# Performance work log

Hardware: AMD Instinct MI355X
Metric: run time of the kernel (lower is better)

## Reference

```python
import jax, jax.numpy as jnp
import numpy as np

N = 40962          # icosphere level-6 vertex count
E = 245772         # N * k (k=6 knn, directed)
MUL_IN = 8         # '8x0e + 8x1o' -> dim 8 + 24 = 32
MUL_OUT = 16       # '16x0e + 16x1o' -> dim 16 + 48 = 64
H = 64             # radial MLP hidden
WNUM = 4 * MUL_IN * MUL_OUT  # 512 per-edge TP weights (4 CG paths)
SQ3 = np.float32(np.sqrt(3.0))


def setup_inputs() -> dict:
    key = jax.random.key(0)
    ks = jax.random.split(key, 8)
    x = jax.random.normal(ks[0], (N, MUL_IN + 3 * MUL_IN), dtype=jnp.float32)
    pos = jax.random.normal(ks[1], (N, 3), dtype=jnp.float32)
    src = jax.random.randint(ks[2], (E,), 0, N)
    dst = jax.random.randint(ks[3], (E,), 0, N)
    edge_index = jnp.stack([src, dst]).astype(jnp.int32)
    W1 = jax.random.normal(ks[4], (1, H), dtype=jnp.float32)
    W2 = jax.random.normal(ks[5], (H, WNUM), dtype=jnp.float32)
    Ws = jax.random.normal(ks[6], (MUL_OUT, MUL_OUT), dtype=jnp.float32)
    k7, k8 = jax.random.split(ks[7])
    Wns = jax.random.normal(k7, (MUL_OUT, MUL_OUT), dtype=jnp.float32)
    Wg = jax.random.normal(k8, (MUL_OUT, MUL_OUT), dtype=jnp.float32)
    return {"x": x, "pos": pos, "edge_index": edge_index,
            "W1": W1, "W2": W2, "Ws": Ws, "Wns": Wns, "Wg": Wg}


def reference(x, pos, edge_index, W1, W2, Ws, Wns, Wg):
    src, dst = edge_index[0], edge_index[1]
    xs = x[:, :MUL_IN]                                  # (N, 8)  scalars (0e)
    xv = x[:, MUL_IN:].reshape(-1, MUL_IN, 3)           # (N, 8, 3) vectors (1o)

    # --- edge geometry + spherical harmonics (component-normalized, lmax=1) ---
    edge_vec = pos[dst] - pos[src]                      # (E, 3)
    edge_len = jnp.maximum(jnp.linalg.norm(edge_vec, axis=-1, keepdims=True), 1e-8)
    edge_dir = edge_vec / edge_len                      # (E, 3)
    Y1 = SQ3 * edge_dir                                 # l=1 SH; l=0 SH == 1

    # --- radial MLP -> per-edge tensor-product weights (shared_weights=False) ---
    h = jax.nn.silu(edge_len @ W1)                      # (E, H), fan_in = 1
    w = (h @ W2) * (1.0 / np.sqrt(np.float32(H)))       # (E, 512)
    wA, wB, wC, wD = [wi.reshape(-1, MUL_IN, MUL_OUT)
                      for wi in jnp.split(w, 4, axis=1)]

    xs_e = xs[src]                                      # (E, 8)   gather
    xv_e = xv[src]                                      # (E, 8, 3) gather
    norm = np.float32(1.0 / np.sqrt(2.0 * MUL_IN))      # path normalization

    # --- tensor product: 4 CG paths ---
    # 0e x 0e -> 0e  (CG = 1)
    pathA = jnp.einsum('eu,euw->ew', xs_e, wA)
    # 1o x 1o -> 0e  (CG_ij = delta_ij / sqrt(3))
    dot = jnp.einsum('eui,ei->eu', xv_e, Y1) * (1.0 / SQ3)
    pathB = jnp.einsum('eu,euw->ew', dot, wB)
    m_s = (pathA + pathB) * norm                        # (E, 16)
    # 0e x 1o -> 1o  (CG = identity)
    pathC = jnp.einsum('eu,euw->ew', xs_e, wC)[:, :, None] * Y1[:, None, :]
    # 1o x 0e -> 1o  (CG = identity)
    pathD = jnp.einsum('eui,euw->ewi', xv_e, wD)
    m_v = (pathC + pathD) * norm                        # (E, 16, 3)

    m = jnp.concatenate([m_s, m_v.reshape(-1, 3 * MUL_OUT)], axis=1)  # (E, 64)

    # --- scatter-add to destination nodes (index_add) ---
    out = jnp.zeros((x.shape[0], m.shape[1]), dtype=x.dtype).at[dst].add(m)

    # --- gated equivariant nonlinearity (o3.Linear with fan-in norm) ---
    lin_norm = np.float32(1.0 / np.sqrt(np.float32(MUL_OUT)))
    os_ = out[:, :MUL_OUT]                              # (N, 16)
    ov_ = out[:, MUL_OUT:].reshape(-1, MUL_OUT, 3)      # (N, 16, 3)
    s = jax.nn.silu(os_ @ Ws * lin_norm)                # (N, 16)
    ns = jnp.einsum('nui,uw->nwi', ov_, Wns) * lin_norm # (N, 16, 3)
    g = jax.nn.sigmoid(os_ @ Wg * lin_norm)             # (N, 16)
    gated = (g[:, :, None] * ns).reshape(-1, 3 * MUL_OUT)
    return jnp.concatenate([s, gated], axis=1)          # (N, 64)
```

## Files before the change

### kernel.cpp

```cpp
#include <hip/hip_runtime.h>
#include <math.h>

typedef _Float16 half8 __attribute__((ext_vector_type(8)));
typedef float floatx4 __attribute__((ext_vector_type(4)));

#define SQ3 1.7320508075688772f

__global__ __launch_bounds__(256) void prep_w2(const float* __restrict__ W2,
                                               _Float16* __restrict__ bw) {
    int t = blockIdx.x * 256 + threadIdx.x;
    if (t >= 32768) return;
    int i    = t & 7;
    int l    = (t >> 3) & 63;
    int s    = (t >> 9) & 1;
    int tt   = (t >> 10) & 7;
    int path = t >> 13;
    int k   = s * 32 + (l >> 4) * 8 + i;
    int col = path * 128 + tt * 16 + (l & 15);
    float scale = 0.03125f * (path == 2 ? SQ3 : 1.0f);
    bw[t] = (_Float16)(W2[k * 512 + col] * scale);
}

struct Pref {
    float4 xa, xb;
    float psx, psy, psz, pdx, pdy, pdz;
    int di;
};

__device__ __forceinline__ Pref issue_loads(int tile, int E,
        const int* __restrict__ ei, const float* __restrict__ x,
        const float* __restrict__ pos, int tid) {
    Pref p;
    int el = tid >> 2, q = tid & 3;
    int eg = tile * 64 + el;
    int ec = (eg < E) ? eg : (E - 1);
    int si = ei[ec];
    p.di = ei[E + ec];
    const float* xr = x + (size_t)si * 32 + q * 8;
    p.xa = *reinterpret_cast<const float4*>(xr);
    p.xb = *reinterpret_cast<const float4*>(xr + 4);
    const float* ps = pos + (size_t)si * 3;
    const float* pd = pos + (size_t)p.di * 3;
    p.psx = ps[0]; p.psy = ps[1]; p.psz = ps[2];
    p.pdx = pd[0]; p.pdy = pd[1]; p.pdz = pd[2];
    return p;
}

__global__ __launch_bounds__(256) void edge_kernel(
    const float* __restrict__ x, const float* __restrict__ pos,
    const int* __restrict__ ei, const float* __restrict__ W1,
    const _Float16* __restrict__ bw, float* __restrict__ out,
    int E, int ntiles)
{
    __shared__ float sW1[64];
    __shared__ __align__(16) float4 s_geo[64];
    __shared__ int s_dst[2][64];
    __shared__ __align__(16) float s_xs[64][12];
    __shared__ __align__(16) float s_xvp[3][64][12];
    __shared__ __align__(16) _Float16 s_hA[4][2][64][8];
    __shared__ __align__(16) _Float16 s_part[2][64][66];

    const int tid  = threadIdx.x;
    const int wave = tid >> 6;
    const int lane = tid & 63;

    if (tid < 64) sW1[tid] = W1[tid];

    half8 bfrag[8][2];
    {
        const half8* bsrc = (const half8*)bw;
        #pragma unroll
        for (int t = 0; t < 8; ++t)
            #pragma unroll
            for (int s = 0; s < 2; ++s)
                bfrag[t][s] = bsrc[(size_t)wave * 1024 + (t * 2 + s) * 64 + lane];
    }

    int tile = blockIdx.x;
    if (tile >= ntiles) return;
    Pref p = issue_loads(tile, E, ei, x, pos, tid);
    __syncthreads();

    int buf = 0;
    for (; tile < ntiles; tile += gridDim.x) {
        {
            int el = tid >> 2, q = tid & 3;
            float ex = p.pdx - p.psx;
            float ey = p.pdy - p.psy;
            float ez = p.pdz - p.psz;
            float len = fmaxf(sqrtf(ex * ex + ey * ey + ez * ez), 1e-8f);
            float inv = 1.0f / len;
            if (q == 0) {
                s_geo[el] = make_float4(ex * inv, ey * inv, ez * inv, len);
                s_dst[buf][el] = p.di;
                *(float4*)&s_xs[el][0] = p.xa;
                *(float4*)&s_xs[el][4] = p.xb;
            } else {
                int fb = (q - 1) * 8;
                float vals[8] = {p.xa.x, p.xa.y, p.xa.z, p.xa.w,
                                 p.xb.x, p.xb.y, p.xb.z, p.xb.w};
                #pragma unroll
                for (int i2 = 0; i2 < 8; ++i2) {
                    int flat = fb + i2;
                    int u  = (flat * 11) >> 5;
                    int ii = flat - 3 * u;
                    s_xvp[ii][el][u] = vals[i2];
                }
            }
            int sub = el >> 4;
            int l   = (q << 4) | (el & 15);
            #pragma unroll
            for (int s = 0; s < 2; ++s) {
                half8 ha;
                #pragma unroll
                for (int i = 0; i < 8; ++i) {
                    float z = len * sW1[s * 32 + q * 8 + i];
                    ha[i] = (_Float16)(z / (1.0f + __expf(-z)));
                }
                *(half8*)&s_hA[sub][s][l][0] = ha;
            }
        }
        __syncthreads();

        int nt = tile + gridDim.x;
        Pref pn;
        if (nt < ntiles) pn = issue_loads(nt, E, ei, x, pos, tid);

        const int wp  = lane & 15;
        const int er0 = (lane >> 4) * 4;
        #pragma unroll
        for (int sub = 0; sub < 4; ++sub) {
            half8 a0 = *(const half8*)&s_hA[sub][0][lane][0];
            half8 a1 = *(const half8*)&s_hA[sub][1][lane][0];
            floatx4 acc[8];
            #pragma unroll
            for (int t = 0; t < 8; ++t) {
                floatx4 z = {0.f, 0.f, 0.f, 0.f};
                z = __builtin_amdgcn_mfma_f32_16x16x32_f16(a0, bfrag[t][0], z, 0, 0, 0);
                acc[t] = __builtin_amdgcn_mfma_f32_16x16x32_f16(a1, bfrag[t][1], z, 0, 0, 0);
            }

            if (wave == 0) {
                #pragma unroll
                for (int r = 0; r < 4; ++r) {
                    int e = sub * 16 + er0 + r;
                    float4 x0 = *(const float4*)&s_xs[e][0];
                    float4 x1 = *(const float4*)&s_xs[e][4];
                    float m = x0.x*acc[0][r] + x0.y*acc[1][r] + x0.z*acc[2][r] + x0.w*acc[3][r]
                            + x1.x*acc[4][r] + x1.y*acc[5][r] + x1.z*acc[6][r] + x1.w*acc[7][r];
                    s_part[0][e][wp] = (_Float16)m;
                }
            } else if (wave == 1) {
                #pragma unroll
                for (int r = 0; r < 4; ++r) {
                    int e = sub * 16 + er0 + r;
                    float4 g = s_geo[e];
                    float m = 0.f;
                    #pragma unroll
                    for (int i = 0; i < 3; ++i) {
                        float4 v0 = *(const float4*)&s_xvp[i][e][0];
                        float4 v1 = *(const float4*)&s_xvp[i][e][4];
                        float gi = (i == 0) ? g.x : ((i == 1) ? g.y : g.z);
                        float d = v0.x*acc[0][r] + v0.y*acc[1][r] + v0.z*acc[2][r] + v0.w*acc[3][r]
                                + v1.x*acc[4][r] + v1.y*acc[5][r] + v1.z*acc[6][r] + v1.w*acc[7][r];
                        m += gi * d;
                    }
                    s_part[1][e][wp] = (_Float16)m;
                }
            } else if (wave == 2) {
                #pragma unroll
                for (int r = 0; r < 4; ++r) {
                    int e = sub * 16 + er0 + r;
                    float4 x0 = *(const float4*)&s_xs[e][0];
                    float4 x1 = *(const float4*)&s_xs[e][4];
                    float4 g = s_geo[e];
                    float cw = x0.x*acc[0][r] + x0.y*acc[1][r] + x0.z*acc[2][r] + x0.w*acc[3][r]
                             + x1.x*acc[4][r] + x1.y*acc[5][r] + x1.z*acc[6][r] + x1.w*acc[7][r];
                    s_part[0][e][16 + wp * 3 + 0] = (_Float16)(cw * g.x);
                    s_part[0][e][16 + wp * 3 + 1] = (_Float16)(cw * g.y);
                    s_part[0][e][16 + wp * 3 + 2] = (_Float16)(cw * g.z);
                }
            } else {
                #pragma unroll
                for (int r = 0; r < 4; ++r) {
                    int e = sub * 16 + er0 + r;
                    #pragma unroll
                    for (int i = 0; i < 3; ++i) {
                        float4 v0 = *(const float4*)&s_xvp[i][e][0];
                        float4 v1 = *(const float4*)&s_xvp[i][e][4];
                        float mi = v0.x*acc[0][r] + v0.y*acc[1][r] + v0.z*acc[2][r] + v0.w*acc[3][r]
                                 + v1.x*acc[4][r] + v1.y*acc[5][r] + v1.z*acc[6][r] + v1.w*acc[7][r];
                        s_part[1][e][16 + wp * 3 + i] = (_Float16)mi;
                    }
                }
            }
        }
        __syncthreads();

        {
            int c = tid & 63;
            int g = tid >> 6;
            #pragma unroll
            for (int k = 0; k < 16; ++k) {
                int e  = g * 16 + k;
                int eg = tile * 64 + e;
                if (eg < E) {
                    float v = (float)s_part[0][e][c] + (float)s_part[1][e][c];
                    atomicAdd(out + (size_t)s_dst[buf][e] * 64 + c, v);
                }
            }
        }
        p = pn;
        buf ^= 1;
    }
}

__global__ __launch_bounds__(256) void node_kernel(
    float* __restrict__ out, const float* __restrict__ Ws,
    const float* __restrict__ Wns, const float* __restrict__ Wg, int N)
{
    int n = blockIdx.x * 256 + threadIdx.x;
    if (n >= N) return;
    float* row = out + (size_t)n * 64;

    float os[16], ov[48];
    #pragma unroll
    for (int q = 0; q < 4; ++q) {
        float4 v = *reinterpret_cast<const float4*>(row + q * 4);
        os[q*4+0]=v.x; os[q*4+1]=v.y; os[q*4+2]=v.z; os[q*4+3]=v.w;
    }
    #pragma unroll
    for (int q = 0; q < 12; ++q) {
        float4 v = *reinterpret_cast<const float4*>(row + 16 + q * 4);
        ov[q*4+0]=v.x; ov[q*4+1]=v.y; ov[q*4+2]=v.z; ov[q*4+3]=v.w;
    }

    float sres[16], gres[16];
    #pragma unroll
    for (int w = 0; w < 16; ++w) {
        float a = 0.f, b = 0.f;
        #pragma unroll
        for (int u = 0; u < 16; ++u) {
            float o_u = os[u];
            a += o_u * Ws[u * 16 + w];
            b += o_u * Wg[u * 16 + w];
        }
        a *= 0.25f; b *= 0.25f;
        sres[w] = a / (1.0f + __expf(-a));
        gres[w] = 1.0f / (1.0f + __expf(-b));
    }

    float gated[48];
    #pragma unroll
    for (int w = 0; w < 16; ++w) {
        float n0 = 0.f, n1 = 0.f, n2 = 0.f;
        #pragma unroll
        for (int u = 0; u < 16; ++u) {
            float wn = Wns[u * 16 + w];
            n0 += ov[u*3+0] * wn;
            n1 += ov[u*3+1] * wn;
            n2 += ov[u*3+2] * wn;
        }
        float gw = gres[w] * 0.25f;
        gated[w*3+0] = n0 * gw;
        gated[w*3+1] = n1 * gw;
        gated[w*3+2] = n2 * gw;
    }

    #pragma unroll
    for (int q = 0; q < 4; ++q) {
        float4 v = make_float4(sres[q*4+0], sres[q*4+1], sres[q*4+2], sres[q*4+3]);
        *reinterpret_cast<float4*>(row + q * 4) = v;
    }
    #pragma unroll
    for (int q = 0; q < 12; ++q) {
        float4 v = make_float4(gated[q*4+0], gated[q*4+1], gated[q*4+2], gated[q*4+3]);
        *reinterpret_cast<float4*>(row + 16 + q * 4) = v;
    }
}

extern "C" void kernel_launch(void* const* d_in, const int* in_sizes, int n_in,
                              void* d_out, int out_size, void* d_ws, size_t ws_size,
                              hipStream_t stream) {
    const float* x   = (const float*)d_in[0];
    const float* pos = (const float*)d_in[1];
    const int*   ei  = (const int*)d_in[2];
    const float* W1  = (const float*)d_in[3];
    const float* W2  = (const float*)d_in[4];
    const float* Ws  = (const float*)d_in[5];
    const float* Wns = (const float*)d_in[6];
    const float* Wg  = (const float*)d_in[7];

    int N = in_sizes[0] / 32;
    int E = in_sizes[2] / 2;
    int ntiles = (E + 63) / 64;
    float* out = (float*)d_out;
    _Float16* bw = (_Float16*)d_ws;

    hipMemsetAsync(out, 0, (size_t)N * 64 * sizeof(float), stream);
    prep_w2<<<128, 256, 0, stream>>>(W2, bw);
    int nblk = ntiles < 1024 ? ntiles : 1024;
    edge_kernel<<<nblk, 256, 0, stream>>>(x, pos, ei, W1, bw, out, E, ntiles);
    node_kernel<<<(N + 255) / 256, 256, 0, stream>>>(out, Ws, Wns, Wg, N);
}
```

Before: 115.1 us.

## Split each TP path across two waves with 512-thread blocks

Doubles the block to 8 waves so each CG path is handled by two waves, each owning half of the input multiplicity (4 of 8 u-channels). This halves the per-wave B-fragment registers and MFMA/epilogue work, and spreads the staging loads over 8 threads per edge. Partial results go into four shared-memory buffers that are summed before the atomic scatter, and the grid is halved to 512 blocks. The cost is extra shared memory and extra partial-sum reads in exchange for more parallelism and lower register pressure per wave.

```diff
diff --git a/kernel.cpp b/kernel.cpp
--- a/kernel.cpp
+++ b/kernel.cpp
@@ -22,7 +22,7 @@
 }
 
 struct Pref {
-    float4 xa, xb;
+    float4 xa;
     float psx, psy, psz, pdx, pdy, pdz;
     int di;
 };
@@ -31,14 +31,12 @@
         const int* __restrict__ ei, const float* __restrict__ x,
         const float* __restrict__ pos, int tid) {
     Pref p;
-    int el = tid >> 2, q = tid & 3;
+    int el = tid >> 3, q = tid & 7;
     int eg = tile * 64 + el;
     int ec = (eg < E) ? eg : (E - 1);
     int si = ei[ec];
     p.di = ei[E + ec];
-    const float* xr = x + (size_t)si * 32 + q * 8;
-    p.xa = *reinterpret_cast<const float4*>(xr);
-    p.xb = *reinterpret_cast<const float4*>(xr + 4);
+    p.xa = *reinterpret_cast<const float4*>(x + (size_t)si * 32 + q * 4);
     const float* ps = pos + (size_t)si * 3;
     const float* pd = pos + (size_t)p.di * 3;
     p.psx = ps[0]; p.psy = ps[1]; p.psz = ps[2];
@@ -46,7 +44,7 @@
     return p;
 }
 
-__global__ __launch_bounds__(256) void edge_kernel(
+__global__ __launch_bounds__(512, 4) void edge_kernel(
     const float* __restrict__ x, const float* __restrict__ pos,
     const int* __restrict__ ei, const float* __restrict__ W1,
     const _Float16* __restrict__ bw, float* __restrict__ out,
@@ -58,22 +56,25 @@
     __shared__ __align__(16) float s_xs[64][12];
     __shared__ __align__(16) float s_xvp[3][64][12];
     __shared__ __align__(16) _Float16 s_hA[4][2][64][8];
-    __shared__ __align__(16) _Float16 s_part[2][64][66];
+    __shared__ __align__(16) _Float16 s_part[4][64][66];
 
     const int tid  = threadIdx.x;
     const int wave = tid >> 6;
+    const int path = wave >> 1;
+    const int th   = wave & 1;
     const int lane = tid & 63;
+    const int ub   = th * 4;
 
     if (tid < 64) sW1[tid] = W1[tid];
 
-    half8 bfrag[8][2];
+    half8 bfrag[4][2];
     {
         const half8* bsrc = (const half8*)bw;
         #pragma unroll
-        for (int t = 0; t < 8; ++t)
+        for (int tt = 0; tt < 4; ++tt)
             #pragma unroll
             for (int s = 0; s < 2; ++s)
-                bfrag[t][s] = bsrc[(size_t)wave * 1024 + (t * 2 + s) * 64 + lane];
+                bfrag[tt][s] = bsrc[(size_t)path * 1024 + ((ub + tt) * 2 + s) * 64 + lane];
     }
 
     int tile = blockIdx.x;
@@ -84,7 +85,7 @@
     int buf = 0;
     for (; tile < ntiles; tile += gridDim.x) {
         {
-            int el = tid >> 2, q = tid & 3;
+            int el = tid >> 3, q = tid & 7;
             float ex = p.pdx - p.psx;
             float ey = p.pdy - p.psy;
             float ez = p.pdz - p.psz;
@@ -93,32 +94,29 @@
             if (q == 0) {
                 s_geo[el] = make_float4(ex * inv, ey * inv, ez * inv, len);
                 s_dst[buf][el] = p.di;
-                *(float4*)&s_xs[el][0] = p.xa;
-                *(float4*)&s_xs[el][4] = p.xb;
+            }
+            if (q < 2) {
+                *(float4*)&s_xs[el][q * 4] = p.xa;
             } else {
-                int fb = (q - 1) * 8;
-                float vals[8] = {p.xa.x, p.xa.y, p.xa.z, p.xa.w,
-                                 p.xb.x, p.xb.y, p.xb.z, p.xb.w};
-                #pragma unroll
-                for (int i2 = 0; i2 < 8; ++i2) {
-                    int flat = fb + i2;
+                float vals[4] = {p.xa.x, p.xa.y, p.xa.z, p.xa.w};
+                #pragma unroll
+                for (int j = 0; j < 4; ++j) {
+                    int flat = (q - 2) * 4 + j;
                     int u  = (flat * 11) >> 5;
                     int ii = flat - 3 * u;
-                    s_xvp[ii][el][u] = vals[i2];
-                }
-            }
+                    s_xvp[ii][el][u] = vals[j];
+                }
+            }
+            int s  = q >> 2, kg = q & 3;
             int sub = el >> 4;
-            int l   = (q << 4) | (el & 15);
-            #pragma unroll
-            for (int s = 0; s < 2; ++s) {
-                half8 ha;
-                #pragma unroll
-                for (int i = 0; i < 8; ++i) {
-                    float z = len * sW1[s * 32 + q * 8 + i];
-                    ha[i] = (_Float16)(z / (1.0f + __expf(-z)));
-                }
-                *(half8*)&s_hA[sub][s][l][0] = ha;
-            }
+            int l   = kg * 16 + (el & 15);
+            half8 ha;
+            #pragma unroll
+            for (int i = 0; i < 8; ++i) {
+                float z = len * sW1[s * 32 + kg * 8 + i];
+                ha[i] = (_Float16)(z / (1.0f + __expf(-z)));
+            }
+            *(half8*)&s_hA[sub][s][l][0] = ha;
         }
         __syncthreads();
 
@@ -132,65 +130,55 @@
         for (int sub = 0; sub < 4; ++sub) {
             half8 a0 = *(const half8*)&s_hA[sub][0][lane][0];
             half8 a1 = *(const half8*)&s_hA[sub][1][lane][0];
-            floatx4 acc[8];
-            #pragma unroll
-            for (int t = 0; t < 8; ++t) {
+            floatx4 acc[4];
+            #pragma unroll
+            for (int tt = 0; tt < 4; ++tt) {
                 floatx4 z = {0.f, 0.f, 0.f, 0.f};
-                z = __builtin_amdgcn_mfma_f32_16x16x32_f16(a0, bfrag[t][0], z, 0, 0, 0);
-                acc[t] = __builtin_amdgcn_mfma_f32_16x16x32_f16(a1, bfrag[t][1], z, 0, 0, 0);
-            }
-
-            if (wave == 0) {
-                #pragma unroll
-                for (int r = 0; r < 4; ++r) {
-                    int e = sub * 16 + er0 + r;
-                    float4 x0 = *(const float4*)&s_xs[e][0];
-                    float4 x1 = *(const float4*)&s_xs[e][4];
-                    float m = x0.x*acc[0][r] + x0.y*acc[1][r] + x0.z*acc[2][r] + x0.w*acc[3][r]
-                            + x1.x*acc[4][r] + x1.y*acc[5][r] + x1.z*acc[6][r] + x1.w*acc[7][r];
-                    s_part[0][e][wp] = (_Float16)m;
-                }
-            } else if (wave == 1) {
+                z = __builtin_amdgcn_mfma_f32_16x16x32_f16(a0, bfrag[tt][0], z, 0, 0, 0);
+                acc[tt] = __builtin_amdgcn_mfma_f32_16x16x32_f16(a1, bfrag[tt][1], z, 0, 0, 0);
+            }
+
+            if (path == 0) {
+                #pragma unroll
+                for (int r = 0; r < 4; ++r) {
+                    int e = sub * 16 + er0 + r;
+                    float4 x0 = *(const float4*)&s_xs[e][ub];
+                    float m = x0.x*acc[0][r] + x0.y*acc[1][r] + x0.z*acc[2][r] + x0.w*acc[3][r];
+                    s_part[th][e][wp] = (_Float16)m;
+                }
+            } else if (path == 1) {
                 #pragma unroll
                 for (int r = 0; r < 4; ++r) {
                     int e = sub * 16 + er0 + r;
                     float4 g = s_geo[e];
-                    float m = 0.f;
+                    float4 v0 = *(const float4*)&s_xvp[0][e][ub];
+                    float4 v1 = *(const float4*)&s_xvp[1][e][ub];
+                    float4 v2 = *(const float4*)&s_xvp[2][e][ub];
+                    float d0 = v0.x*acc[0][r] + v0.y*acc[1][r] + v0.z*acc[2][r] + v0.w*acc[3][r];
+                    float d1 = v1.x*acc[0][r] + v1.y*acc[1][r] + v1.z*acc[2][r] + v1.w*acc[3][r];
+                    float d2 = v2.x*acc[0][r] + v2.y*acc[1][r] + v2.z*acc[2][r] + v2.w*acc[3][r];
+                    s_part[2 + th][e][wp] = (_Float16)(g.x*d0 + g.y*d1 + g.z*d2);
+                }
+            } else if (path == 2) {
+                #pragma unroll
+                for (int r = 0; r < 4; ++r) {
+                    int e = sub * 16 + er0 + r;
+                    float4 x0 = *(const float4*)&s_xs[e][ub];
+                    float4 g = s_geo[e];
+                    float cw = x0.x*acc[0][r] + x0.y*acc[1][r] + x0.z*acc[2][r] + x0.w*acc[3][r];
+                    s_part[th][e][16 + wp * 3 + 0] = (_Float16)(cw * g.x);
+                    s_part[th][e][16 + wp * 3 + 1] = (_Float16)(cw * g.y);
+                    s_part[th][e][16 + wp * 3 + 2] = (_Float16)(cw * g.z);
+                }
+            } else {
+                #pragma unroll
+                for (int r = 0; r < 4; ++r) {
+                    int e = sub * 16 + er0 + r;
                     #pragma unroll
                     for (int i = 0; i < 3; ++i) {
-                        float4 v0 = *(const float4*)&s_xvp[i][e][0];
-                        float4 v1 = *(const float4*)&s_xvp[i][e][4];
-                        float gi = (i == 0) ? g.x : ((i == 1) ? g.y : g.z);
-                        float d = v0.x*acc[0][r] + v0.y*acc[1][r] + v0.z*acc[2][r] + v0.w*acc[3][r]
-                                + v1.x*acc[4][r] + v1.y*acc[5][r] + v1.z*acc[6][r] + v1.w*acc[7][r];
-                        m += gi * d;
-                    }
-                    s_part[1][e][wp] = (_Float16)m;
-                }
-            } else if (wave == 2) {
-                #pragma unroll
-                for (int r = 0; r < 4; ++r) {
-                    int e = sub * 16 + er0 + r;
-                    float4 x0 = *(const float4*)&s_xs[e][0];
-                    float4 x1 = *(const float4*)&s_xs[e][4];
-                    float4 g = s_geo[e];
-                    float cw = x0.x*acc[0][r] + x0.y*acc[1][r] + x0.z*acc[2][r] + x0.w*acc[3][r]
-                             + x1.x*acc[4][r] + x1.y*acc[5][r] + x1.z*acc[6][r] + x1.w*acc[7][r];
-                    s_part[0][e][16 + wp * 3 + 0] = (_Float16)(cw * g.x);
-                    s_part[0][e][16 + wp * 3 + 1] = (_Float16)(cw * g.y);
-                    s_part[0][e][16 + wp * 3 + 2] = (_Float16)(cw * g.z);
-                }
-            } else {
-                #pragma unroll
-                for (int r = 0; r < 4; ++r) {
-                    int e = sub * 16 + er0 + r;
-                    #pragma unroll
-                    for (int i = 0; i < 3; ++i) {
-                        float4 v0 = *(const float4*)&s_xvp[i][e][0];
-                        float4 v1 = *(const float4*)&s_xvp[i][e][4];
-                        float mi = v0.x*acc[0][r] + v0.y*acc[1][r] + v0.z*acc[2][r] + v0.w*acc[3][r]
-                                 + v1.x*acc[4][r] + v1.y*acc[5][r] + v1.z*acc[6][r] + v1.w*acc[7][r];
-                        s_part[1][e][16 + wp * 3 + i] = (_Float16)mi;
+                        float4 v0 = *(const float4*)&s_xvp[i][e][ub];
+                        float mi = v0.x*acc[0][r] + v0.y*acc[1][r] + v0.z*acc[2][r] + v0.w*acc[3][r];
+                        s_part[2 + th][e][16 + wp * 3 + i] = (_Float16)mi;
                     }
                 }
             }
@@ -201,11 +189,12 @@
             int c = tid & 63;
             int g = tid >> 6;
             #pragma unroll
-            for (int k = 0; k < 16; ++k) {
-                int e  = g * 16 + k;
+            for (int k = 0; k < 8; ++k) {
+                int e  = g * 8 + k;
                 int eg = tile * 64 + e;
                 if (eg < E) {
-                    float v = (float)s_part[0][e][c] + (float)s_part[1][e][c];
+                    float v = (float)s_part[0][e][c] + (float)s_part[1][e][c]
+                            + (float)s_part[2][e][c] + (float)s_part[3][e][c];
                     atomicAdd(out + (size_t)s_dst[buf][e] * 64 + c, v);
                 }
             }
@@ -299,7 +288,7 @@
 
     hipMemsetAsync(out, 0, (size_t)N * 64 * sizeof(float), stream);
     prep_w2<<<128, 256, 0, stream>>>(W2, bw);
-    int nblk = ntiles < 1024 ? ntiles : 1024;
-    edge_kernel<<<nblk, 256, 0, stream>>>(x, pos, ei, W1, bw, out, E, ntiles);
+    int nblk = ntiles < 512 ? ntiles : 512;
+    edge_kernel<<<nblk, 512, 0, stream>>>(x, pos, ei, W1, bw, out, E, ntiles);
     node_kernel<<<(N + 255) / 256, 256, 0, stream>>>(out, Ws, Wns, Wg, N);
 }
```

New measurement: 107.8 us. -6.4%, faster.
